# Performance work log

Measured on AMD Instinct MI355X. Metric: run time of the kernel, lower is better.

The kernel has to match this reference:

```python
import jax, jax.numpy as jnp
import numpy as np

EPS = 1e-06


def setup_inputs() -> dict:
    key = jax.random.key(0)
    k1, k2 = jax.random.split(key)
    x = jax.random.normal(k1, (8, 128, 256, 256), dtype=jnp.float32)
    weights = jax.random.normal(k2, (128,), dtype=jnp.float32)
    return {"x": x, "weights": weights}


def reference(x, weights):
    # x: [b, q, h, w]; weights: [q]
    q = weights.shape[0]
    norm_const = jnp.float32(q)
    # use_cumsum=False path: softmax over features, scaled by norm_const
    wt = jax.nn.softmax(weights) * norm_const  # [q]
    # rank[b,i,h,w] = rank of x[b,i,h,w] when sorting dim 1 descending
    order = jnp.argsort(-x, axis=1)            # descending argsort
    rank = jnp.argsort(order, axis=1)          # inverse permutation -> ranks
    # gather per-rank weight and apply 1/sqrt(x^2 + eps)
    return wt[rank] * jax.lax.rsqrt(x * x + jnp.float32(EPS))
```

## Files before the change

kernel.cpp:

```cpp
#include <hip/hip_runtime.h>
#include <math.h>


#define Q    128
#define TCOL 64
#define HW   65536
#define EPSF 1e-6f

__launch_bounds__(256, 4)
__global__ void rank_weight_kernel(const float* __restrict__ x,
                                   const float* __restrict__ weights,
                                   float* __restrict__ out) {
    __shared__ float lds_x[Q][TCOL];
    __shared__ float lds_wt[Q];

    const int tid = threadIdx.x;
    const int g   = blockIdx.x;
    const int b   = g >> 10;
    const int hw0 = (g & 1023) << 6;
    const float* xb = x   + (size_t)b * Q * HW + hw0;
    float*       ob = out + (size_t)b * Q * HW + hw0;

    for (int f = tid; f < Q * (TCOL / 4); f += 256) {
        const int r = f >> 4;
        const int p = f & 15;
        float4 val = *reinterpret_cast<const float4*>(xb + (size_t)r * HW + (p << 2));
        *reinterpret_cast<float4*>(&lds_x[r][p << 2]) = val;
    }

    if (tid < 64) {
        float w0 = weights[tid];
        float w1 = weights[tid + 64];
        float m = fmaxf(w0, w1);
        #pragma unroll
        for (int off = 32; off; off >>= 1) m = fmaxf(m, __shfl_xor(m, off, 64));
        float e0 = __expf(w0 - m), e1 = __expf(w1 - m);
        float s = e0 + e1;
        #pragma unroll
        for (int off = 32; off; off >>= 1) s += __shfl_xor(s, off, 64);
        float scale = 128.0f / s;
        lds_wt[tid]      = e0 * scale;
        lds_wt[tid + 64] = e1 * scale;
    }
    __syncthreads();

    const int wave = tid >> 6;
    const int c    = tid & 63;

    for (int ci = 0; ci < 4; ++ci) {
        const int i0 = wave * 32 + ci * 8;

        float v[8];
        #pragma unroll
        for (int u = 0; u < 8; ++u) v[u] = lds_x[i0 + u][c];
        int rk[8];
        #pragma unroll
        for (int u = 0; u < 8; ++u) rk[u] = 0;

        for (int j = 0; j < i0; j += 8) {
            #pragma unroll
            for (int jj = 0; jj < 8; ++jj) {
                float w = lds_x[j + jj][c];
                #pragma unroll
                for (int u = 0; u < 8; ++u) rk[u] += (w >= v[u]);
            }
        }
        #pragma unroll
        for (int ju = 0; ju < 8; ++ju) {
            #pragma unroll
            for (int u = 0; u < 8; ++u) {
                if (ju < u)      rk[u] += (v[ju] >= v[u]);
                else if (ju > u) rk[u] += (v[ju] >  v[u]);
            }
        }
        for (int j = i0 + 8; j < Q; j += 8) {
            #pragma unroll
            for (int jj = 0; jj < 8; ++jj) {
                float w = lds_x[j + jj][c];
                #pragma unroll
                for (int u = 0; u < 8; ++u) rk[u] += (w > v[u]);
            }
        }

        #pragma unroll
        for (int u = 0; u < 8; ++u) {
            float wt  = lds_wt[rk[u]];
            float val = v[u];
            ob[(size_t)(i0 + u) * HW + c] = wt * rsqrtf(val * val + EPSF);
        }
    }
}

extern "C" void kernel_launch(void* const* d_in, const int* in_sizes, int n_in,
                              void* d_out, int out_size, void* d_ws, size_t ws_size,
                              hipStream_t stream) {
    const float* x  = (const float*)d_in[0];
    const float* wt = (const float*)d_in[1];
    float* out      = (float*)d_out;

    dim3 grid(8192), block(256);
    hipLaunchKernelGGL(rank_weight_kernel, grid, block, 0, stream, x, wt, out);
}
```

Measured before the change: 786.2 us.

## Register-block 32 rows per thread with pairwise symmetric compares and inline-asm carry accumulation

Each thread now holds all 32 of its rows in registers instead of 8 at a time. Each neighbour value loaded from LDS is therefore reused 32 times, and the intra-block ranks use a symmetric pairwise compare: one compare updates both elements, one by add-with-carry and one by subtract-with-borrow. Inline asm turns each compare plus increment into v_cmp and v_addc, so no separate cndmask/add is needed. This cuts LDS reads and the ALU instruction count. The cost is much higher VGPR pressure against the launch bounds of 4 blocks, and the inline asm relies on hand-managed SGPR carry pairs.

```diff
diff --git a/kernel.cpp b/kernel.cpp
--- a/kernel.cpp
+++ b/kernel.cpp
@@ -6,6 +6,23 @@
 #define TCOL 64
 #define HW   65536
 #define EPSF 1e-6f
+
+__device__ __forceinline__ void acc_ge(int& rk, float a, float b) {
+    unsigned long long c, dead;
+    asm("v_cmp_ge_f32 %0, %1, %2" : "=s"(c) : "v"(a), "v"(b));
+    asm("v_addc_co_u32 %0, %1, %0, 0, %2" : "+v"(rk), "=s"(dead) : "s"(c));
+}
+__device__ __forceinline__ void acc_gt(int& rk, float a, float b) {
+    unsigned long long c, dead;
+    asm("v_cmp_gt_f32 %0, %1, %2" : "=s"(c) : "v"(a), "v"(b));
+    asm("v_addc_co_u32 %0, %1, %0, 0, %2" : "+v"(rk), "=s"(dead) : "s"(c));
+}
+__device__ __forceinline__ void pair_upd(int& rkb, int& rka, float va, float vb) {
+    unsigned long long c, d1, d2;
+    asm("v_cmp_ge_f32 %0, %1, %2" : "=s"(c) : "v"(va), "v"(vb));
+    asm("v_addc_co_u32 %0, %1, %0, 0, %2" : "+v"(rkb), "=s"(d1) : "s"(c));
+    asm("v_subb_co_u32 %0, %1, %0, 0, %2" : "+v"(rka), "=s"(d2) : "s"(c));
+}
 
 __launch_bounds__(256, 4)
 __global__ void rank_weight_kernel(const float* __restrict__ x,
@@ -46,48 +63,43 @@
 
     const int wave = tid >> 6;
     const int c    = tid & 63;
+    const int R0   = wave * 32;
 
-    for (int ci = 0; ci < 4; ++ci) {
-        const int i0 = wave * 32 + ci * 8;
+    float v[32];
+    int   rk[32];
+    #pragma unroll
+    for (int u = 0; u < 32; ++u) v[u] = lds_x[R0 + u][c];
+    #pragma unroll
+    for (int u = 0; u < 32; ++u) rk[u] = 31 - u;
 
-        float v[8];
+    #pragma unroll
+    for (int a = 0; a < 32; ++a) {
         #pragma unroll
-        for (int u = 0; u < 8; ++u) v[u] = lds_x[i0 + u][c];
-        int rk[8];
+        for (int bq = a + 1; bq < 32; ++bq) pair_upd(rk[bq], rk[a], v[a], v[bq]);
+    }
+
+    for (int j = 0; j < R0; j += 2) {
+        float w0 = lds_x[j][c];
+        float w1 = lds_x[j + 1][c];
         #pragma unroll
-        for (int u = 0; u < 8; ++u) rk[u] = 0;
+        for (int u = 0; u < 32; ++u) acc_ge(rk[u], w0, v[u]);
+        #pragma unroll
+        for (int u = 0; u < 32; ++u) acc_ge(rk[u], w1, v[u]);
+    }
+    for (int j = R0 + 32; j < Q; j += 2) {
+        float w0 = lds_x[j][c];
+        float w1 = lds_x[j + 1][c];
+        #pragma unroll
+        for (int u = 0; u < 32; ++u) acc_gt(rk[u], w0, v[u]);
+        #pragma unroll
+        for (int u = 0; u < 32; ++u) acc_gt(rk[u], w1, v[u]);
+    }
 
-        for (int j = 0; j < i0; j += 8) {
-            #pragma unroll
-            for (int jj = 0; jj < 8; ++jj) {
-                float w = lds_x[j + jj][c];
-                #pragma unroll
-                for (int u = 0; u < 8; ++u) rk[u] += (w >= v[u]);
-            }
-        }
-        #pragma unroll
-        for (int ju = 0; ju < 8; ++ju) {
-            #pragma unroll
-            for (int u = 0; u < 8; ++u) {
-                if (ju < u)      rk[u] += (v[ju] >= v[u]);
-                else if (ju > u) rk[u] += (v[ju] >  v[u]);
-            }
-        }
-        for (int j = i0 + 8; j < Q; j += 8) {
-            #pragma unroll
-            for (int jj = 0; jj < 8; ++jj) {
-                float w = lds_x[j + jj][c];
-                #pragma unroll
-                for (int u = 0; u < 8; ++u) rk[u] += (w > v[u]);
-            }
-        }
-
-        #pragma unroll
-        for (int u = 0; u < 8; ++u) {
-            float wt  = lds_wt[rk[u]];
-            float val = v[u];
-            ob[(size_t)(i0 + u) * HW + c] = wt * rsqrtf(val * val + EPSF);
-        }
+    #pragma unroll
+    for (int u = 0; u < 32; ++u) {
+        float wt  = lds_wt[rk[u]];
+        float val = v[u];
+        ob[(size_t)(R0 + u) * HW + c] = wt * rsqrtf(val * val + EPSF);
     }
 }
 
```

Result: no change. 772.8 us (-1.7%).
